# Performance work log

Measured on AMD Instinct MI355X. Metric: run time of the kernel, lower is better.

The kernel has to match this reference:

```python
import jax, jax.numpy as jnp
import numpy as np

D_MODEL = 4096
N_Q_HEADS = 32
N_KV_HEADS = 8
HEAD_DIM = D_MODEL // N_Q_HEADS  # 128
N_REP = N_Q_HEADS // N_KV_HEADS  # 4
BATCH = 2
SEQ = 2048
ROPE_THETA = 10000.0


def setup_inputs() -> dict:
    key = jax.random.key(0)
    ks = jax.random.split(key, 5)
    scale = 0.02
    x = jax.random.normal(ks[0], (BATCH, SEQ, D_MODEL), dtype=jnp.float32)
    w_q = jax.random.normal(ks[1], (D_MODEL, N_Q_HEADS * HEAD_DIM), dtype=jnp.float32) * scale
    w_k = jax.random.normal(ks[2], (D_MODEL, N_KV_HEADS * HEAD_DIM), dtype=jnp.float32) * scale
    w_v = jax.random.normal(ks[3], (D_MODEL, N_KV_HEADS * HEAD_DIM), dtype=jnp.float32) * scale
    w_o = jax.random.normal(ks[4], (N_Q_HEADS * HEAD_DIM, D_MODEL), dtype=jnp.float32) * scale
    # precompute_theta_pos_freqs: freqs_cis = exp(1j * outer(t, inv_freq))
    inv_freq = 1.0 / (ROPE_THETA ** (jnp.arange(0, HEAD_DIM, 2)[: HEAD_DIM // 2] / HEAD_DIM))
    t = jnp.arange(SEQ, dtype=jnp.float32)
    freqs = jnp.outer(t, inv_freq)  # [S, HEAD_DIM//2]
    freqs_cos = jnp.cos(freqs).astype(jnp.float32)
    freqs_sin = jnp.sin(freqs).astype(jnp.float32)
    # additive causal mask [1,1,S,S]
    causal = jnp.tril(jnp.ones((SEQ, SEQ), dtype=bool))
    mask = jnp.where(causal, 0.0, -1e9).astype(jnp.float32)[None, None]
    return {"x": x, "w_q": w_q, "w_k": w_k, "w_v": w_v, "w_o": w_o,
            "freqs_cos": freqs_cos, "freqs_sin": freqs_sin, "mask": mask}


def _apply_rope(t, cos, sin):
    # t: [B,S,H,D]; cos/sin: [S,D//2]. Complex multiply in real arithmetic:
    # (a + bi) * (c + di) = (ac - bd) + (ad + bc)i
    B, S, H, D = t.shape
    tr = t.reshape(B, S, H, D // 2, 2)
    a, b = tr[..., 0], tr[..., 1]
    c = cos[None, :, None, :]
    s = sin[None, :, None, :]
    out = jnp.stack([a * c - b * s, a * s + b * c], axis=-1)
    return out.reshape(B, S, H, D)


def reference(x, w_q, w_k, w_v, w_o, freqs_cos, freqs_sin, mask):
    B, S, _ = x.shape
    xq = (x @ w_q).reshape(B, S, N_Q_HEADS, HEAD_DIM)
    xk = (x @ w_k).reshape(B, S, N_KV_HEADS, HEAD_DIM)
    xv = (x @ w_v).reshape(B, S, N_KV_HEADS, HEAD_DIM)
    xq = _apply_rope(xq, freqs_cos, freqs_sin)
    xk = _apply_rope(xk, freqs_cos, freqs_sin)
    # repeat_kv (tile+reshape == repeat along head axis)
    keys = jnp.repeat(xk, N_REP, axis=2)    # [B,S,Hq,D]
    values = jnp.repeat(xv, N_REP, axis=2)  # [B,S,Hq,D]
    xq = xq.transpose(0, 2, 1, 3)           # [B,Hq,S,D]
    keys = keys.transpose(0, 2, 1, 3)
    values = values.transpose(0, 2, 1, 3)
    scores = jnp.einsum("bhqd,bhkd->bhqk", xq, keys) / jnp.sqrt(
        jnp.asarray(HEAD_DIM, dtype=xq.dtype))
    scores = scores + mask
    probs = jax.nn.softmax(scores, axis=-1).astype(xq.dtype)
    out = jnp.einsum("bhqk,bhkd->bhqd", probs, values)
    out = out.transpose(0, 2, 1, 3).reshape(B, S, N_Q_HEADS * HEAD_DIM)
    return out @ w_o


if __name__ == "__main__":
    inp = setup_inputs()
    y = reference(**inp)
    print(y.shape, y.dtype)
```

## Files before the change

### kernel.cpp

```cpp
#include <hip/hip_runtime.h>
#include <stdint.h>
#include <stddef.h>


typedef __bf16 bf16x8 __attribute__((ext_vector_type(8)));
typedef float floatx4 __attribute__((ext_vector_type(4)));
typedef unsigned short ushort8v __attribute__((ext_vector_type(8)));
typedef unsigned short ushort4v __attribute__((ext_vector_type(4)));
typedef unsigned short ushort2v __attribute__((ext_vector_type(2)));

#define DEV static __device__ __forceinline__

DEV unsigned short f2bf(float f) {
  union { float f; unsigned u; } v; v.f = f;
  unsigned r = v.u + 0x7fffu + ((v.u >> 16) & 1u);
  return (unsigned short)(r >> 16);
}
DEV float bf2f(unsigned short b) {
  union { unsigned u; float f; } v; v.u = ((unsigned)b) << 16;
  return v.f;
}

DEV void gload_lds16(const void* g, void* lds) {
  __builtin_amdgcn_global_load_lds(
      (__attribute__((address_space(1))) void*)(g),
      (__attribute__((address_space(3))) void*)(lds), 16, 0, 0);
}

__global__ __launch_bounds__(256) void cvt_fp32_bf16(
    const float* __restrict__ in, unsigned short* __restrict__ out, int n4) {
  int i = blockIdx.x * 256 + threadIdx.x;
  if (i >= n4) return;
  float4 v = ((const float4*)in)[i];
  ushort4v w;
  w.x = f2bf(v.x); w.y = f2bf(v.y); w.z = f2bf(v.z); w.w = f2bf(v.w);
  *(ushort4v*)(out + (size_t)i * 4) = w;
}

__global__ __launch_bounds__(256) void transpose_cvt(
    const float* __restrict__ in, unsigned short* __restrict__ out, int K, int N) {
  __shared__ float tile[32][33];
  int k0 = blockIdx.x * 32, n0 = blockIdx.y * 32;
  int tx = threadIdx.x & 31, ty = threadIdx.x >> 5;
  for (int i = 0; i < 32; i += 8)
    tile[ty + i][tx] = in[(size_t)(k0 + ty + i) * N + n0 + tx];
  __syncthreads();
  for (int i = 0; i < 32; i += 8)
    out[(size_t)(n0 + ty + i) * K + k0 + tx] = f2bf(tile[tx][ty + i]);
}

#define LD8(LDS, D, ROW, Q)                                                  \
  (*(const bf16x8*)((const char*)(LDS) + (D) * 32768 + (ROW) * 128 +         \
                    (((Q) ^ ((ROW) & 7)) << 4)))

#define STAGE(PANEL, LDS, KT, H)                                             \
  {                                                                          \
    _Pragma("unroll") for (int j_ = 0; j_ < 2; ++j_) {                       \
      int t_ = wave * 2 + j_;                                                \
      int row_ = (H) * 128 + t_ * 8 + srow;                                  \
      gload_lds16(PANEL + (size_t)row_ * K + (size_t)(KT) * 64 + qsrc * 8,   \
                  (char*)(LDS) + ((KT) & 1) * 32768 + (H) * 16384 +          \
                      t_ * 1024);                                            \
    }                                                                        \
  }

#define READ_A(D, MH)                                                        \
  _Pragma("unroll") for (int mf_ = 0; mf_ < 4; ++mf_)                        \
      _Pragma("unroll") for (int kk_ = 0; kk_ < 2; ++kk_)                    \
          aR[mf_][kk_] =                                                     \
      LD8(a_lds, D, wm + ((MH) * 4 + mf_) * 16 + l16, kk_ * 4 + quad);

#define READ_B(D, NH, BREG)                                                  \
  _Pragma("unroll") for (int nf_ = 0; nf_ < 2; ++nf_)                        \
      _Pragma("unroll") for (int kk_ = 0; kk_ < 2; ++kk_)                    \
          BREG[nf_][kk_] =                                                   \
      LD8(b_lds, D, wn + ((NH) * 2 + nf_) * 16 + l16, kk_ * 4 + quad);

#define MFMA_Q(MH, NH, BREG)                                                 \
  _Pragma("unroll") for (int mf_ = 0; mf_ < 4; ++mf_)                        \
      _Pragma("unroll") for (int nf_ = 0; nf_ < 2; ++nf_)                    \
          _Pragma("unroll") for (int kk_ = 0; kk_ < 2; ++kk_)                \
              acc[(MH) * 4 + mf_][(NH) * 2 + nf_] =                          \
      __builtin_amdgcn_mfma_f32_16x16x32_bf16(                               \
          aR[mf_][kk_], BREG[nf_][kk_],                                      \
          acc[(MH) * 4 + mf_][(NH) * 2 + nf_], 0, 0, 0);

#define PH_SYNC_BEGIN                                                        \
  __builtin_amdgcn_s_barrier();                                              \
  asm volatile("s_waitcnt lgkmcnt(0)" ::: "memory");                         \
  __builtin_amdgcn_s_setprio(1);

#define PH_SYNC_END                                                          \
  __builtin_amdgcn_s_setprio(0);                                             \
  __builtin_amdgcn_s_barrier();

template <int STORE_F32>
__global__ __launch_bounds__(512, 2) void gemm_bt8(
    const unsigned short* __restrict__ A, const unsigned short* __restrict__ Bt,
    void* __restrict__ Cp, int M, int N, int K) {
  __shared__ __align__(16) unsigned short a_lds[32768];
  __shared__ __align__(16) unsigned short b_lds[32768];

  const int tid = threadIdx.x;
  const int wave = tid >> 6, lane = tid & 63;
  const int quad = lane >> 4, l16 = lane & 15;
  const int wm = (wave >> 2) * 128, wn = (wave & 3) * 64;

  const int gx = gridDim.x, gy = gridDim.y;
  int lid = blockIdx.y * gx + blockIdx.x;
  int cpx = (gx * gy) >> 3;
  int swz = (lid & 7) * cpx + (lid >> 3);
  const int m0 = (swz / gy) * 256, n0 = (swz % gy) * 256;

  const int qsrc = (lane & 7) ^ (lane >> 3);
  const int srow = lane >> 3;
  const unsigned short* Ab = A + (size_t)m0 * K;
  const unsigned short* Bb = Bt + (size_t)n0 * K;

  floatx4 acc[8][4] = {};
  bf16x8 aR[4][2], bLo[2][2], bHi[2][2];

  const int nt = K >> 6;
  const int iters = nt >> 1;

  STAGE(Ab, a_lds, 0, 0); STAGE(Ab, a_lds, 0, 1);
  STAGE(Bb, b_lds, 0, 0); STAGE(Bb, b_lds, 0, 1);
  STAGE(Bb, b_lds, 1, 0); STAGE(Bb, b_lds, 1, 1);
  asm volatile("s_waitcnt vmcnt(0)" ::: "memory");
  __builtin_amdgcn_s_barrier();

  for (int i = 0; i < iters; ++i) {
    const int t0 = 2 * i;
    const bool has2 = (t0 + 2 < nt);
    READ_A(0, 0); READ_B(0, 0, bLo);
    STAGE(Ab, a_lds, t0 + 1, 0);
    PH_SYNC_BEGIN; MFMA_Q(0, 0, bLo); PH_SYNC_END;
    READ_B(0, 1, bHi);
    STAGE(Ab, a_lds, t0 + 1, 1);
    PH_SYNC_BEGIN; MFMA_Q(0, 1, bHi); PH_SYNC_END;
    READ_A(0, 1);
    if (has2) STAGE(Bb, b_lds, t0 + 2, 0);
    PH_SYNC_BEGIN; MFMA_Q(1, 1, bHi); PH_SYNC_END;
    if (has2) {
      STAGE(Bb, b_lds, t0 + 2, 1);
      asm volatile("s_waitcnt vmcnt(4)" ::: "memory");
    } else {
      asm volatile("s_waitcnt vmcnt(0)" ::: "memory");
    }
    PH_SYNC_BEGIN; MFMA_Q(1, 0, bLo); PH_SYNC_END;
    READ_A(1, 0); READ_B(1, 0, bLo);
    if (has2) STAGE(Ab, a_lds, t0 + 2, 0);
    PH_SYNC_BEGIN; MFMA_Q(0, 0, bLo); PH_SYNC_END;
    READ_B(1, 1, bHi);
    if (has2) STAGE(Ab, a_lds, t0 + 2, 1);
    PH_SYNC_BEGIN; MFMA_Q(0, 1, bHi); PH_SYNC_END;
    READ_A(1, 1);
    if (has2) STAGE(Bb, b_lds, t0 + 3, 0);
    PH_SYNC_BEGIN; MFMA_Q(1, 1, bHi); PH_SYNC_END;
    if (has2) {
      STAGE(Bb, b_lds, t0 + 3, 1);
      asm volatile("s_waitcnt vmcnt(4)" ::: "memory");
    } else {
      asm volatile("s_waitcnt vmcnt(0)" ::: "memory");
    }
    PH_SYNC_BEGIN; MFMA_Q(1, 0, bLo); PH_SYNC_END;
  }

#pragma unroll
  for (int mf = 0; mf < 8; ++mf)
#pragma unroll
    for (int nf = 0; nf < 4; ++nf)
#pragma unroll
      for (int r = 0; r < 4; ++r) {
        int row = m0 + wm + mf * 16 + quad * 4 + r;
        int col = n0 + wn + nf * 16 + l16;
        float v = acc[mf][nf][r];
        if (STORE_F32)
          ((float*)Cp)[(size_t)row * N + col] = v;
        else
          ((unsigned short*)Cp)[(size_t)row * N + col] = f2bf(v);
      }
}

__global__ __launch_bounds__(256) void rope_q(
    const unsigned short* __restrict__ qkv, const float* __restrict__ fc,
    const float* __restrict__ fs, unsigned short* __restrict__ Qd) {
  int gid = blockIdx.x * 256 + threadIdx.x;
  int i = gid & 63;
  int h = (gid >> 6) & 31;
  int s = (gid >> 11) & 2047;
  int b = gid >> 22;
  int row = b * 2048 + s;
  ushort2v p = *(const ushort2v*)(qkv + (size_t)row * 6144 + h * 128 + 2 * i);
  float a = bf2f(p.x), bb = bf2f(p.y);
  float c = fc[s * 64 + i], sn = fs[s * 64 + i];
  ushort2v w;
  w.x = f2bf(a * c - bb * sn);
  w.y = f2bf(a * sn + bb * c);
  *(ushort2v*)(Qd + ((((size_t)b * 32 + h) * 2048 + s) * 128 + 2 * i)) = w;
}

__global__ __launch_bounds__(256) void rope_k(
    const unsigned short* __restrict__ qkv, const float* __restrict__ fc,
    const float* __restrict__ fs, unsigned short* __restrict__ Kd) {
  int gid = blockIdx.x * 256 + threadIdx.x;
  int i = gid & 63;
  int kvh = (gid >> 6) & 7;
  int s = (gid >> 9) & 2047;
  int b = gid >> 20;
  int row = b * 2048 + s;
  ushort2v p = *(const ushort2v*)(qkv + (size_t)row * 6144 + 4096 + kvh * 128 + 2 * i);
  float a = bf2f(p.x), bb = bf2f(p.y);
  float c = fc[s * 64 + i], sn = fs[s * 64 + i];
  ushort2v w;
  w.x = f2bf(a * c - bb * sn);
  w.y = f2bf(a * sn + bb * c);
  *(ushort2v*)(Kd + ((((size_t)b * 8 + kvh) * 2048 + s) * 128 + 2 * i)) = w;
}

__global__ __launch_bounds__(256) void vtrans(
    const unsigned short* __restrict__ qkv, unsigned short* __restrict__ Vt) {
  __shared__ unsigned short tile[32][33];
  int bk = blockIdx.z;
  int b = bk >> 3, kvh = bk & 7;
  int s0 = blockIdx.x * 32, d0 = blockIdx.y * 32;
  int tx = threadIdx.x & 31, ty = threadIdx.x >> 5;
  for (int i = 0; i < 32; i += 8)
    tile[ty + i][tx] =
        qkv[(size_t)(b * 2048 + s0 + ty + i) * 6144 + 5120 + kvh * 128 + d0 + tx];
  __syncthreads();
  for (int i = 0; i < 32; i += 8)
    Vt[((size_t)bk * 128 + d0 + ty + i) * 2048 + s0 + tx] = tile[tx][ty + i];
}

__global__ __launch_bounds__(512, 4) void attn_kernel(
    const unsigned short* __restrict__ Q,
    const unsigned short* __restrict__ Kd,
    const unsigned short* __restrict__ Vt,
    unsigned short* __restrict__ O) {
  __shared__ __align__(16) unsigned short k_lds[64][136];
  __shared__ __align__(16) unsigned short v_lds[128][72];
  __shared__ __align__(16) unsigned short p_lds[8][16][72];

  const int tid = threadIdx.x;
  const int wave = tid >> 6, lane = tid & 63;
  const int quad = lane >> 4, l16 = lane & 15;
  const int pr = blockIdx.x;
  const int h = blockIdx.y;
  const int b = blockIdx.z;
  const int kvh = h >> 2;
  const float scale = 0.08838834764831845f;

  const unsigned short* kbase = Kd + ((size_t)b * 8 + kvh) * 2048 * 128;
  const unsigned short* vbase = Vt + ((size_t)b * 8 + kvh) * 128 * 2048;

  const int kk = tid >> 4, kd = tid & 15;
  const int vd = tid >> 3, vs = tid & 7;

  for (int pass = 0; pass < 2; ++pass) {
    const int qt = pass == 0 ? pr : 15 - pr;
    const int q0 = qt * 128;

    const unsigned short* qrow =
        Q + (((size_t)b * 32 + h) * 2048 + q0 + wave * 16 + l16) * 128;
    bf16x8 qf[4];
    for (int t = 0; t < 4; ++t)
      qf[t] = *(const bf16x8*)(qrow + t * 32 + quad * 8);

    float m_i[4], l_i[4];
    for (int r = 0; r < 4; ++r) { m_i[r] = -3.0e38f; l_i[r] = 0.f; }
    floatx4 o_acc[8] = {};

    ushort8v krg[2], vrg[2];
    krg[0] = *(const ushort8v*)(kbase + (size_t)kk * 128 + kd * 8);
    krg[1] = *(const ushort8v*)(kbase + (size_t)(kk + 32) * 128 + kd * 8);
    vrg[0] = *(const ushort8v*)(vbase + (size_t)vd * 2048 + vs * 8);
    vrg[1] = *(const ushort8v*)(vbase + (size_t)(vd + 64) * 2048 + vs * 8);

    const int kb_last = q0 + 64;
    for (int kb = 0; kb <= kb_last; kb += 64) {
      __syncthreads();
      *(ushort8v*)&k_lds[kk][kd * 8] = krg[0];
      *(ushort8v*)&k_lds[kk + 32][kd * 8] = krg[1];
      *(ushort8v*)&v_lds[vd][vs * 8] = vrg[0];
      *(ushort8v*)&v_lds[vd + 64][vs * 8] = vrg[1];
      __syncthreads();
      if (kb < kb_last) {
        int nkb = kb + 64;
        krg[0] = *(const ushort8v*)(kbase + (size_t)(nkb + kk) * 128 + kd * 8);
        krg[1] = *(const ushort8v*)(kbase + (size_t)(nkb + kk + 32) * 128 + kd * 8);
        vrg[0] = *(const ushort8v*)(vbase + (size_t)vd * 2048 + nkb + vs * 8);
        vrg[1] = *(const ushort8v*)(vbase + (size_t)(vd + 64) * 2048 + nkb + vs * 8);
      }
      if (kb > q0 + wave * 16 + 15) continue;

      float sv[4][4];
      for (int kt = 0; kt < 4; ++kt) {
        floatx4 a = {0.f, 0.f, 0.f, 0.f};
        for (int t = 0; t < 4; ++t) {
          bf16x8 kf = *(const bf16x8*)&k_lds[kt * 16 + l16][t * 32 + quad * 8];
          a = __builtin_amdgcn_mfma_f32_16x16x32_bf16(qf[t], kf, a, 0, 0, 0);
        }
        for (int r = 0; r < 4; ++r) sv[kt][r] = a[r] * scale;
      }
      if (kb + 63 > q0 + wave * 16) {
        for (int kt = 0; kt < 4; ++kt) {
          int kcol = kb + kt * 16 + l16;
          for (int r = 0; r < 4; ++r) {
            int qg = q0 + wave * 16 + quad * 4 + r;
            if (kcol > qg) sv[kt][r] -= 1.0e9f;
          }
        }
      }
      float mx[4];
      for (int r = 0; r < 4; ++r) {
        float m = fmaxf(fmaxf(sv[0][r], sv[1][r]), fmaxf(sv[2][r], sv[3][r]));
        for (int off = 1; off < 16; off <<= 1)
          m = fmaxf(m, __shfl_xor(m, off));
        mx[r] = m;
      }
      bool grow = false;
      for (int r = 0; r < 4; ++r) grow |= (mx[r] > m_i[r] + 8.f);
      if (__any(grow)) {
        for (int r = 0; r < 4; ++r) {
          float mnew = fmaxf(m_i[r], mx[r]);
          float alpha = __expf(m_i[r] - mnew);
          m_i[r] = mnew;
          l_i[r] *= alpha;
          for (int nb = 0; nb < 8; ++nb) o_acc[nb][r] *= alpha;
        }
      }
      for (int r = 0; r < 4; ++r) {
        float sum = 0.f;
        for (int kt = 0; kt < 4; ++kt) {
          float p = __expf(sv[kt][r] - m_i[r]);
          sv[kt][r] = p;
          sum += p;
        }
        for (int off = 1; off < 16; off <<= 1)
          sum += __shfl_xor(sum, off);
        l_i[r] += sum;
      }
      for (int kt = 0; kt < 4; ++kt)
        for (int r = 0; r < 4; ++r)
          p_lds[wave][quad * 4 + r][kt * 16 + l16] = f2bf(sv[kt][r]);
      for (int tk = 0; tk < 2; ++tk) {
        bf16x8 pa = *(const bf16x8*)&p_lds[wave][l16][tk * 32 + quad * 8];
        for (int nb = 0; nb < 8; ++nb) {
          bf16x8 vb = *(const bf16x8*)&v_lds[nb * 16 + l16][tk * 32 + quad * 8];
          o_acc[nb] = __builtin_amdgcn_mfma_f32_16x16x32_bf16(pa, vb, o_acc[nb], 0, 0, 0);
        }
      }
    }

    for (int nb = 0; nb < 8; ++nb)
      for (int r = 0; r < 4; ++r) {
        int row = b * 2048 + q0 + wave * 16 + quad * 4 + r;
        int col = h * 128 + nb * 16 + l16;
        O[(size_t)row * 4096 + col] = f2bf(o_acc[nb][r] / l_i[r]);
      }
  }
}

extern "C" void kernel_launch(void* const* d_in, const int* in_sizes, int n_in,
                              void* d_out, int out_size, void* d_ws, size_t ws_size,
                              hipStream_t stream) {
  const float* x   = (const float*)d_in[0];
  const float* w_q = (const float*)d_in[1];
  const float* w_k = (const float*)d_in[2];
  const float* w_v = (const float*)d_in[3];
  const float* w_o = (const float*)d_in[4];
  const float* fc  = (const float*)d_in[5];
  const float* fs  = (const float*)d_in[6];
  (void)in_sizes; (void)n_in; (void)out_size; (void)ws_size;

  char* ws = (char*)d_ws;
  unsigned short* xb  = (unsigned short*)(ws);
  unsigned short* wT  = (unsigned short*)(ws + 33554432ull);
  unsigned short* qkv = (unsigned short*)(ws + 83886080ull);
  unsigned short* Kd  = (unsigned short*)(ws + 134217728ull);
  unsigned short* Vt  = (unsigned short*)(ws + 142606336ull);
  unsigned short* Qd  = xb;
  unsigned short* woT = wT;
  unsigned short* Ob  = qkv;

  cvt_fp32_bf16<<<16384, 256, 0, stream>>>(x, xb, 4194304);
  transpose_cvt<<<dim3(128, 128), 256, 0, stream>>>(w_q, wT, 4096, 4096);
  transpose_cvt<<<dim3(128, 32), 256, 0, stream>>>(w_k, wT + (size_t)4096 * 4096, 4096, 1024);
  transpose_cvt<<<dim3(128, 32), 256, 0, stream>>>(w_v, wT + (size_t)5120 * 4096, 4096, 1024);
  gemm_bt8<0><<<dim3(16, 24), 512, 0, stream>>>(xb, wT, qkv, 4096, 6144, 4096);
  transpose_cvt<<<dim3(128, 128), 256, 0, stream>>>(w_o, woT, 4096, 4096);
  rope_q<<<32768, 256, 0, stream>>>(qkv, fc, fs, Qd);
  rope_k<<<8192, 256, 0, stream>>>(qkv, fc, fs, Kd);
  vtrans<<<dim3(64, 4, 16), 256, 0, stream>>>(qkv, Vt);
  attn_kernel<<<dim3(8, 32, 2), 512, 0, stream>>>(Qd, Kd, Vt, Ob);
  gemm_bt8<1><<<dim3(16, 16), 512, 0, stream>>>(Ob, woT, d_out, 4096, 4096, 4096);
}
```

Before: 794.3 us.

## Software-pipeline LDS reads across iterations and remap tiles per XCD

Moves the first LDS fragment reads of each iteration into the previous iteration's tail so that LDS reads overlap MFMA work. It also adds sched_barrier fences around the waits and reorders the barriers. Separately, the block-to-tile mapping now gives each XCD a contiguous 2D region (split in halves along M and quarters along N) to improve L2 reuse of A and B tiles. The new mapping assumes gx is divisible by 2 and gy by 4, and the extra barriers add synchronisation overhead.

Result: no change. 796.4 us (+0.3%).

```diff
diff --git a/kernel.cpp b/kernel.cpp
--- a/kernel.cpp
+++ b/kernel.cpp
@@ -85,14 +85,15 @@
           aR[mf_][kk_], BREG[nf_][kk_],                                      \
           acc[(MH) * 4 + mf_][(NH) * 2 + nf_], 0, 0, 0);
 
-#define PH_SYNC_BEGIN                                                        \
-  __builtin_amdgcn_s_barrier();                                              \
+#define BAR __builtin_amdgcn_s_barrier()
+#define SCHED0 __builtin_amdgcn_sched_barrier(0)
+#define WAITL0                                                               \
   asm volatile("s_waitcnt lgkmcnt(0)" ::: "memory");                         \
-  __builtin_amdgcn_s_setprio(1);
-
-#define PH_SYNC_END                                                          \
-  __builtin_amdgcn_s_setprio(0);                                             \
-  __builtin_amdgcn_s_barrier();
+  SCHED0
+#define VMC4 asm volatile("s_waitcnt vmcnt(4)" ::: "memory")
+#define VMC0 asm volatile("s_waitcnt vmcnt(0)" ::: "memory")
+#define PRIO1 __builtin_amdgcn_s_setprio(1)
+#define PRIO0 __builtin_amdgcn_s_setprio(0)
 
 template <int STORE_F32>
 __global__ __launch_bounds__(512, 2) void gemm_bt8(
@@ -108,9 +109,11 @@
 
   const int gx = gridDim.x, gy = gridDim.y;
   int lid = blockIdx.y * gx + blockIdx.x;
-  int cpx = (gx * gy) >> 3;
-  int swz = (lid & 7) * cpx + (lid >> 3);
-  const int m0 = (swz / gy) * 256, n0 = (swz % gy) * 256;
+  int xcd = lid & 7, idx = lid >> 3;
+  int gm = gx >> 1, gn = gy >> 2;
+  int xm = xcd & 1, xn = xcd >> 1;
+  const int m0 = (xm * gm + idx % gm) * 256;
+  const int n0 = (xn * gn + idx / gm) * 256;
 
   const int qsrc = (lane & 7) ^ (lane >> 3);
   const int srow = lane >> 3;
@@ -118,7 +121,7 @@
   const unsigned short* Bb = Bt + (size_t)n0 * K;
 
   floatx4 acc[8][4] = {};
-  bf16x8 aR[4][2], bLo[2][2], bHi[2][2];
+  bf16x8 aR[4][2], bL[2][2], bH[2][2];
 
   const int nt = K >> 6;
   const int iters = nt >> 1;
@@ -126,44 +129,52 @@
   STAGE(Ab, a_lds, 0, 0); STAGE(Ab, a_lds, 0, 1);
   STAGE(Bb, b_lds, 0, 0); STAGE(Bb, b_lds, 0, 1);
   STAGE(Bb, b_lds, 1, 0); STAGE(Bb, b_lds, 1, 1);
-  asm volatile("s_waitcnt vmcnt(0)" ::: "memory");
-  __builtin_amdgcn_s_barrier();
+  VMC0;
+  BAR;
+  READ_A(0, 0); READ_B(0, 0, bL);
 
   for (int i = 0; i < iters; ++i) {
     const int t0 = 2 * i;
     const bool has2 = (t0 + 2 < nt);
-    READ_A(0, 0); READ_B(0, 0, bLo);
     STAGE(Ab, a_lds, t0 + 1, 0);
-    PH_SYNC_BEGIN; MFMA_Q(0, 0, bLo); PH_SYNC_END;
-    READ_B(0, 1, bHi);
+    BAR; WAITL0;
+    PRIO1; MFMA_Q(0, 0, bL); PRIO0;
+    READ_B(0, 1, bH);
+    BAR;
     STAGE(Ab, a_lds, t0 + 1, 1);
-    PH_SYNC_BEGIN; MFMA_Q(0, 1, bHi); PH_SYNC_END;
+    BAR; WAITL0;
+    PRIO1; MFMA_Q(0, 1, bH); PRIO0;
     READ_A(0, 1);
+    BAR;
     if (has2) STAGE(Bb, b_lds, t0 + 2, 0);
-    PH_SYNC_BEGIN; MFMA_Q(1, 1, bHi); PH_SYNC_END;
-    if (has2) {
-      STAGE(Bb, b_lds, t0 + 2, 1);
-      asm volatile("s_waitcnt vmcnt(4)" ::: "memory");
-    } else {
-      asm volatile("s_waitcnt vmcnt(0)" ::: "memory");
-    }
-    PH_SYNC_BEGIN; MFMA_Q(1, 0, bLo); PH_SYNC_END;
-    READ_A(1, 0); READ_B(1, 0, bLo);
+    BAR; WAITL0;
+    PRIO1; MFMA_Q(1, 1, bH); PRIO0;
+    BAR;
+    if (has2) { STAGE(Bb, b_lds, t0 + 2, 1); VMC4; } else { VMC0; }
+    BAR; SCHED0;
+    PRIO1; MFMA_Q(1, 0, bL); PRIO0;
+    READ_A(1, 0);
+    READ_B(1, 0, bL);
+    BAR;
     if (has2) STAGE(Ab, a_lds, t0 + 2, 0);
-    PH_SYNC_BEGIN; MFMA_Q(0, 0, bLo); PH_SYNC_END;
-    READ_B(1, 1, bHi);
+    BAR; WAITL0;
+    PRIO1; MFMA_Q(0, 0, bL); PRIO0;
+    READ_B(1, 1, bH);
+    BAR;
     if (has2) STAGE(Ab, a_lds, t0 + 2, 1);
-    PH_SYNC_BEGIN; MFMA_Q(0, 1, bHi); PH_SYNC_END;
+    BAR; WAITL0;
+    PRIO1; MFMA_Q(0, 1, bH); PRIO0;
     READ_A(1, 1);
+    BAR;
     if (has2) STAGE(Bb, b_lds, t0 + 3, 0);
-    PH_SYNC_BEGIN; MFMA_Q(1, 1, bHi); PH_SYNC_END;
-    if (has2) {
-      STAGE(Bb, b_lds, t0 + 3, 1);
-      asm volatile("s_waitcnt vmcnt(4)" ::: "memory");
-    } else {
-      asm volatile("s_waitcnt vmcnt(0)" ::: "memory");
-    }
-    PH_SYNC_BEGIN; MFMA_Q(1, 0, bLo); PH_SYNC_END;
+    BAR; WAITL0;
+    PRIO1; MFMA_Q(1, 1, bH); PRIO0;
+    BAR;
+    if (has2) { STAGE(Bb, b_lds, t0 + 3, 1); VMC4; } else { VMC0; }
+    BAR; SCHED0;
+    PRIO1; MFMA_Q(1, 0, bL); PRIO0;
+    if (i + 1 < iters) { READ_A(0, 0); READ_B(0, 0, bL); }
+    BAR;
   }
 
 #pragma unroll
```
